# Kernel optimization log

Measured on AMD Instinct MI355X. Metric: run time of the kernel, lower is better.

## Reference

```python
import jax, jax.numpy as jnp
import numpy as np

N_NODES = 100000
N_EDGES = 1600000
IN_DIM = 128
HID = 32
HEADS = 4
OUT_DIM = 40
NEG_SLOPE = 0.2
BN_EPS = 1e-5


def setup_inputs() -> dict:
    key = jax.random.key(0)
    ks = jax.random.split(key, 13)
    x = jax.random.normal(ks[0], (N_NODES, IN_DIM), jnp.float32)
    edge_index = jax.random.randint(ks[1], (2, N_EDGES), 0, N_NODES, dtype=jnp.int32)
    s0 = 1.0 / np.sqrt(IN_DIM)
    s1 = 1.0 / np.sqrt(HEADS * HID)
    return {
        "x": x,
        "edge_index": edge_index,
        # layer 0: GATConv(IN_DIM -> HID, HEADS heads, concat)
        "W0": jax.random.normal(ks[2], (IN_DIM, HEADS * HID), jnp.float32) * s0,
        "a_src0": jax.random.normal(ks[3], (HEADS, HID), jnp.float32) * s0,
        "a_dst0": jax.random.normal(ks[4], (HEADS, HID), jnp.float32) * s0,
        "b0": jnp.zeros((HEADS * HID,), jnp.float32),
        # BatchNorm1d(HEADS*HID)
        "gamma0": jnp.ones((HEADS * HID,), jnp.float32),
        "beta0": jnp.zeros((HEADS * HID,), jnp.float32),
        # layer 1: GATConv(HEADS*HID -> OUT_DIM, 1 head, mean)
        "W1": jax.random.normal(ks[5], (HEADS * HID, OUT_DIM), jnp.float32) * s1,
        "a_src1": jax.random.normal(ks[6], (1, OUT_DIM), jnp.float32) * s1,
        "a_dst1": jax.random.normal(ks[7], (1, OUT_DIM), jnp.float32) * s1,
        "b1": jnp.zeros((OUT_DIM,), jnp.float32),
    }


def gat_conv(x, src, dst, n_nodes, W, a_src, a_dst, b, heads, concat):
    # linear transform: [N, H, C]
    h = (x @ W).reshape(n_nodes, heads, -1)
    # per-node attention logits [N, H]
    alpha_src = (h * a_src).sum(-1)
    alpha_dst = (h * a_dst).sum(-1)
    # per-edge raw attention [E, H]
    e = jax.nn.leaky_relu(alpha_src[src] + alpha_dst[dst], NEG_SLOPE)
    # softmax over incoming edges of each destination node
    m = jax.ops.segment_max(e, dst, num_segments=n_nodes)  # self-loops -> no empty segment
    ex = jnp.exp(e - m[dst])
    den = jax.ops.segment_sum(ex, dst, num_segments=n_nodes)
    # weighted scatter-aggregate of messages [E, H, C] -> [N, H, C]
    out = jax.ops.segment_sum(ex[:, :, None] * h[src], dst, num_segments=n_nodes)
    out = out / den[:, :, None]
    out = out.reshape(n_nodes, -1) if concat else out.mean(axis=1)
    return out + b


def batch_norm(x, gamma, beta):
    mu = x.mean(axis=0)
    var = x.var(axis=0)
    return (x - mu) * jax.lax.rsqrt(var + BN_EPS) * gamma + beta


def reference(x, edge_index, W0, a_src0, a_dst0, b0, gamma0, beta0,
              W1, a_src1, a_dst1, b1):
    n = x.shape[0]
    loop = jnp.arange(n, dtype=edge_index.dtype)
    src = jnp.concatenate([edge_index[0], loop])  # add self-loops (PyG default)
    dst = jnp.concatenate([edge_index[1], loop])
    # layer 0: GATConv -> BN -> ELU (dropout p=0 / eval -> identity)
    h = gat_conv(x, src, dst, n, W0, a_src0, a_dst0, b0, HEADS, True)
    h = jax.nn.elu(batch_norm(h, gamma0, beta0))
    # layer 1: GATConv, 1 head, mean aggregation, no BN/act
    out = gat_conv(h, src, dst, n, W1, a_src1, a_dst1, b1, 1, False)
    return out
```

## Files before the change

### kernel.cpp

```cpp
#include <hip/hip_runtime.h>
#include <hip/hip_bf16.h>
#include <math.h>

#define NN   100000
#define EE   1600000
#define ETOT (NN + EE)
#define IND  128
#define HD   128
#define OD   40
#define NEG  0.2f
#define BNEPS 1e-5f
#define NBKT 16

typedef __attribute__((ext_vector_type(8))) short bf16x8;
typedef __attribute__((ext_vector_type(4))) float f32x4;

__device__ __forceinline__ float lrelu(float x) { return x > 0.f ? x : NEG * x; }

__device__ __forceinline__ unsigned pack_bf16(float a, float b) {
  unsigned ua = __float_as_uint(a), ub = __float_as_uint(b);
  ua = (ua + 0x7fffu + ((ua >> 16) & 1u)) >> 16;
  ub = (ub + 0x7fffu + ((ub >> 16) & 1u)) >> 16;
  return ua | (ub << 16);
}
__device__ __forceinline__ float bf16_lo(unsigned v) { return __uint_as_float(v << 16); }
__device__ __forceinline__ float bf16_hi(unsigned v) { return __uint_as_float(v & 0xffff0000u); }

__global__ void prep_kernel(const float* __restrict__ W0, unsigned* __restrict__ w0t,
                            const int* __restrict__ ei, int* __restrict__ deg,
                            int* __restrict__ rank) {
  int gid = blockIdx.x * blockDim.x + threadIdx.x;
  if (gid < 128 * 64) {
    int n = gid & 127, kp = gid >> 7;
    float lo = W0[(size_t)(2 * kp) * 128 + n];
    float hi = W0[(size_t)(2 * kp + 1) * 128 + n];
    w0t[n * 64 + kp] = pack_bf16(lo, hi);
  }
  int i8 = gid * 8;
  if (i8 >= ETOT) return;
  int4 dA, dB;
  if (i8 < EE) {
    dA = *(const int4*)&ei[EE + i8];
    dB = *(const int4*)&ei[EE + i8 + 4];
  } else {
    int b = i8 - EE;
    dA = make_int4(b, b + 1, b + 2, b + 3);
    dB = make_int4(b + 4, b + 5, b + 6, b + 7);
  }
  int4 rA, rB;
  rA.x = atomicAdd(&deg[dA.x], 1);
  rA.y = atomicAdd(&deg[dA.y], 1);
  rA.z = atomicAdd(&deg[dA.z], 1);
  rA.w = atomicAdd(&deg[dA.w], 1);
  rB.x = atomicAdd(&deg[dB.x], 1);
  rB.y = atomicAdd(&deg[dB.y], 1);
  rB.z = atomicAdd(&deg[dB.z], 1);
  rB.w = atomicAdd(&deg[dB.w], 1);
  *(int4*)&rank[i8] = rA;
  *(int4*)&rank[i8 + 4] = rB;
}

__global__ __launch_bounds__(256) void gemm0_kernel(const float* __restrict__ x,
                                                    const unsigned* __restrict__ w0t,
                                                    const float* __restrict__ a_src0,
                                                    const float* __restrict__ a_dst0,
                                                    unsigned* __restrict__ h0b,
                                                    float* __restrict__ asrc0,
                                                    float* __restrict__ adst0) {
  __shared__ __align__(16) unsigned As[64][68];
  __shared__ __align__(16) unsigned Wt[128][68];
  int t = threadIdx.x;
  int rowbase = blockIdx.x * 64;
  for (int idx = t; idx < 128 * 64; idx += 256) {
    Wt[idx >> 6][idx & 63] = w0t[idx];
  }
  for (int idx = t; idx < 64 * 64; idx += 256) {
    int row = idx >> 6, kp = idx & 63;
    int r = rowbase + row;
    int rc = r < NN ? r : NN - 1;
    float2 v = *(const float2*)&x[(size_t)rc * 128 + kp * 2];
    As[row][kp] = pack_bf16(v.x, v.y);
  }
  __syncthreads();

  int lane = t & 63, w = t >> 6;
  int mrow = lane & 15, g = lane >> 4;
  f32x4 acc[8];
#pragma unroll
  for (int nt = 0; nt < 8; nt++) acc[nt] = (f32x4){0.f, 0.f, 0.f, 0.f};
#pragma unroll
  for (int ks = 0; ks < 4; ks++) {
    bf16x8 a = *(const bf16x8*)&As[w * 16 + mrow][ks * 16 + g * 4];
#pragma unroll
    for (int nt = 0; nt < 8; nt++) {
      bf16x8 b = *(const bf16x8*)&Wt[nt * 16 + mrow][ks * 16 + g * 4];
      acc[nt] = __builtin_amdgcn_mfma_f32_16x16x32_bf16(a, b, acc[nt], 0, 0, 0);
    }
  }
  int col = lane & 15;
  float as_[8], ad_[8];
#pragma unroll
  for (int nt = 0; nt < 8; nt++) {
    as_[nt] = a_src0[nt * 16 + col];
    ad_[nt] = a_dst0[nt * 16 + col];
  }
#pragma unroll
  for (int reg = 0; reg < 4; reg++) {
    int r = rowbase + w * 16 + g * 4 + reg;
    bool rok = r < NN;
    float hs0 = acc[0][reg] * as_[0] + acc[1][reg] * as_[1];
    float hs1 = acc[2][reg] * as_[2] + acc[3][reg] * as_[3];
    float hs2 = acc[4][reg] * as_[4] + acc[5][reg] * as_[5];
    float hs3 = acc[6][reg] * as_[6] + acc[7][reg] * as_[7];
    float hd0 = acc[0][reg] * ad_[0] + acc[1][reg] * ad_[1];
    float hd1 = acc[2][reg] * ad_[2] + acc[3][reg] * ad_[3];
    float hd2 = acc[4][reg] * ad_[4] + acc[5][reg] * ad_[5];
    float hd3 = acc[6][reg] * ad_[6] + acc[7][reg] * ad_[7];
#pragma unroll
    for (int mk = 1; mk < 16; mk <<= 1) {
      hs0 += __shfl_xor(hs0, mk); hs1 += __shfl_xor(hs1, mk);
      hs2 += __shfl_xor(hs2, mk); hs3 += __shfl_xor(hs3, mk);
      hd0 += __shfl_xor(hd0, mk); hd1 += __shfl_xor(hd1, mk);
      hd2 += __shfl_xor(hd2, mk); hd3 += __shfl_xor(hd3, mk);
    }
    if ((lane & 15) == 0 && rok) {
      asrc0[r * 4 + 0] = hs0; asrc0[r * 4 + 1] = hs1;
      asrc0[r * 4 + 2] = hs2; asrc0[r * 4 + 3] = hs3;
      adst0[r * 4 + 0] = hd0; adst0[r * 4 + 1] = hd1;
      adst0[r * 4 + 2] = hd2; adst0[r * 4 + 3] = hd3;
    }
#pragma unroll
    for (int nt = 0; nt < 8; nt++) {
      float v = acc[nt][reg];
      float nv = __shfl_xor(v, 1);
      if (!(col & 1) && rok) h0b[(size_t)r * 64 + nt * 8 + (col >> 1)] = pack_bf16(v, nv);
    }
  }
}

__global__ __launch_bounds__(256) void scanA_kernel(const int* __restrict__ deg,
                                                    int* __restrict__ scanned,
                                                    int* __restrict__ blocksums) {
  __shared__ int s[256];
  int t = threadIdx.x;
  int i = blockIdx.x * 256 + t;
  int v = (i < NN) ? deg[i] : 0;
  s[t] = v;
  __syncthreads();
  for (int off = 1; off < 256; off <<= 1) {
    int add = (t >= off) ? s[t - off] : 0;
    __syncthreads();
    s[t] += add;
    __syncthreads();
  }
  if (i < NN) scanned[i] = s[t];
  if (t == 255) blocksums[blockIdx.x] = s[255];
}

__global__ __launch_bounds__(512) void scanB_kernel(int* __restrict__ blocksums, int NB) {
  __shared__ int s[512];
  int t = threadIdx.x;
  int v = (t < NB) ? blocksums[t] : 0;
  s[t] = v;
  __syncthreads();
  for (int off = 1; off < 512; off <<= 1) {
    int add = (t >= off) ? s[t - off] : 0;
    __syncthreads();
    s[t] += add;
    __syncthreads();
  }
  if (t < NB) blocksums[t] = s[t] - v;
}

__global__ __launch_bounds__(256) void scanC_kernel(const int* __restrict__ scanned,
                                                    const int* __restrict__ deg,
                                                    const int* __restrict__ blocksums,
                                                    int* __restrict__ rowptr) {
  int i = blockIdx.x * 256 + threadIdx.x;
  if (i < NN) rowptr[i] = blocksums[blockIdx.x] + scanned[i] - deg[i];
  if (i == 0) rowptr[NN] = ETOT;
}

__global__ void scatter_kernel(const int* __restrict__ ei, const int* __restrict__ rowptr,
                               const int* __restrict__ rank, int* __restrict__ csr_src) {
  int i8 = (blockIdx.x * blockDim.x + threadIdx.x) * 8;
  if (i8 >= ETOT) return;
  int4 sA, dA, sB, dB;
  if (i8 < EE) {
    sA = *(const int4*)&ei[i8];
    sB = *(const int4*)&ei[i8 + 4];
    dA = *(const int4*)&ei[EE + i8];
    dB = *(const int4*)&ei[EE + i8 + 4];
  } else {
    int b = i8 - EE;
    sA = make_int4(b, b + 1, b + 2, b + 3);
    sB = make_int4(b + 4, b + 5, b + 6, b + 7);
    dA = sA; dB = sB;
  }
  int4 rA = *(const int4*)&rank[i8];
  int4 rB = *(const int4*)&rank[i8 + 4];
  int p0 = rowptr[dA.x] + rA.x;
  int p1 = rowptr[dA.y] + rA.y;
  int p2 = rowptr[dA.z] + rA.z;
  int p3 = rowptr[dA.w] + rA.w;
  int p4 = rowptr[dB.x] + rB.x;
  int p5 = rowptr[dB.y] + rB.y;
  int p6 = rowptr[dB.z] + rB.z;
  int p7 = rowptr[dB.w] + rB.w;
  csr_src[p0] = sA.x;
  csr_src[p1] = sA.y;
  csr_src[p2] = sA.z;
  csr_src[p3] = sA.w;
  csr_src[p4] = sB.x;
  csr_src[p5] = sB.y;
  csr_src[p6] = sB.z;
  csr_src[p7] = sB.w;
}

__global__ __launch_bounds__(256) void agg0_kernel(const int* __restrict__ csr_src,
                                                   const int* __restrict__ rowptr,
                                                   const float* __restrict__ asrc0,
                                                   const float* __restrict__ adst0,
                                                   const unsigned* __restrict__ h0b,
                                                   const float* __restrict__ b0,
                                                   unsigned* __restrict__ agg0b,
                                                   float* __restrict__ bnsumB,
                                                   float* __restrict__ bnsqB) {
  __shared__ float ws[16][4][17];
  __shared__ int   ss[16][16];
  __shared__ float Lsum[4][16][8], Lsq[4][16][8];
  int t = threadIdx.x;
  int grp = t >> 4;
  int p   = t & 15;
  int n = blockIdx.x * 16 + grp;
  int start = rowptr[n], end = rowptr[n + 1];
  float4 ad = *(const float4*)&adst0[(size_t)n * 4];
  int head = p >> 2;
  float a0 = 0.f, a1 = 0.f, a2 = 0.f, a3 = 0.f, a4 = 0.f, a5 = 0.f, a6 = 0.f, a7 = 0.f;
  float d0 = 0.f, d1 = 0.f, d2 = 0.f, d3 = 0.f;

  for (int base = start; base < end; base += 16) {
    int cnt = min(16, end - base);
    if (p < cnt) {
      int s = csr_src[base + p];
      float4 as = *(const float4*)&asrc0[(size_t)s * 4];
      float w0 = __expf(lrelu(as.x + ad.x));
      float w1 = __expf(lrelu(as.y + ad.y));
      float w2 = __expf(lrelu(as.z + ad.z));
      float w3 = __expf(lrelu(as.w + ad.w));
      d0 += w0; d1 += w1; d2 += w2; d3 += w3;
      ss[grp][p] = s;
      ws[grp][0][p] = w0;
      ws[grp][1][p] = w1;
      ws[grp][2][p] = w2;
      ws[grp][3][p] = w3;
    }
    __builtin_amdgcn_wave_barrier();
    for (int eb = 0; eb < cnt; eb += 4) {
      int e0 = eb, e1 = eb + 1, e2 = eb + 2, e3 = eb + 3;
      float w0 = ws[grp][head][e0];
      float w1 = (e1 < cnt) ? ws[grp][head][e1] : 0.f;
      float w2 = (e2 < cnt) ? ws[grp][head][e2] : 0.f;
      float w3 = (e3 < cnt) ? ws[grp][head][e3] : 0.f;
      int s0 = ss[grp][e0];
      int s1 = ss[grp][(e1 < cnt) ? e1 : e0];
      int s2 = ss[grp][(e2 < cnt) ? e2 : e0];
      int s3 = ss[grp][(e3 < cnt) ? e3 : e0];
      uint4 h0v = *(const uint4*)&h0b[(size_t)s0 * 64 + p * 4];
      uint4 h1v = *(const uint4*)&h0b[(size_t)s1 * 64 + p * 4];
      uint4 h2v = *(const uint4*)&h0b[(size_t)s2 * 64 + p * 4];
      uint4 h3v = *(const uint4*)&h0b[(size_t)s3 * 64 + p * 4];
      a0 += w0 * bf16_lo(h0v.x); a1 += w0 * bf16_hi(h0v.x);
      a2 += w0 * bf16_lo(h0v.y); a3 += w0 * bf16_hi(h0v.y);
      a4 += w0 * bf16_lo(h0v.z); a5 += w0 * bf16_hi(h0v.z);
      a6 += w0 * bf16_lo(h0v.w); a7 += w0 * bf16_hi(h0v.w);
      a0 += w1 * bf16_lo(h1v.x); a1 += w1 * bf16_hi(h1v.x);
      a2 += w1 * bf16_lo(h1v.y); a3 += w1 * bf16_hi(h1v.y);
      a4 += w1 * bf16_lo(h1v.z); a5 += w1 * bf16_hi(h1v.z);
      a6 += w1 * bf16_lo(h1v.w); a7 += w1 * bf16_hi(h1v.w);
      a0 += w2 * bf16_lo(h2v.x); a1 += w2 * bf16_hi(h2v.x);
      a2 += w2 * bf16_lo(h2v.y); a3 += w2 * bf16_hi(h2v.y);
      a4 += w2 * bf16_lo(h2v.z); a5 += w2 * bf16_hi(h2v.z);
      a6 += w2 * bf16_lo(h2v.w); a7 += w2 * bf16_hi(h2v.w);
      a0 += w3 * bf16_lo(h3v.x); a1 += w3 * bf16_hi(h3v.x);
      a2 += w3 * bf16_lo(h3v.y); a3 += w3 * bf16_hi(h3v.y);
      a4 += w3 * bf16_lo(h3v.z); a5 += w3 * bf16_hi(h3v.z);
      a6 += w3 * bf16_lo(h3v.w); a7 += w3 * bf16_hi(h3v.w);
    }
    __builtin_amdgcn_wave_barrier();
  }
#pragma unroll
  for (int mk = 1; mk < 16; mk <<= 1) {
    d0 += __shfl_xor(d0, mk);
    d1 += __shfl_xor(d1, mk);
    d2 += __shfl_xor(d2, mk);
    d3 += __shfl_xor(d3, mk);
  }
  float dh = head == 0 ? d0 : head == 1 ? d1 : head == 2 ? d2 : d3;
  float rd = 1.f / dh;
  int c = p * 8;
  float4 b1v = *(const float4*)&b0[c];
  float4 b2v = *(const float4*)&b0[c + 4];
  float o0 = a0 * rd + b1v.x, o1 = a1 * rd + b1v.y;
  float o2 = a2 * rd + b1v.z, o3 = a3 * rd + b1v.w;
  float o4 = a4 * rd + b2v.x, o5 = a5 * rd + b2v.y;
  float o6 = a6 * rd + b2v.z, o7 = a7 * rd + b2v.w;
  uint4 o;
  o.x = pack_bf16(o0, o1);
  o.y = pack_bf16(o2, o3);
  o.z = pack_bf16(o4, o5);
  o.w = pack_bf16(o6, o7);
  *(uint4*)&agg0b[(size_t)n * 64 + p * 4] = o;

  float s0 = o0, s1 = o1, s2 = o2, s3 = o3, s4 = o4, s5 = o5, s6 = o6, s7 = o7;
  float q0 = o0 * o0, q1 = o1 * o1, q2 = o2 * o2, q3 = o3 * o3;
  float q4 = o4 * o4, q5 = o5 * o5, q6 = o6 * o6, q7 = o7 * o7;
#pragma unroll
  for (int mk = 16; mk < 64; mk <<= 1) {
    s0 += __shfl_xor(s0, mk); s1 += __shfl_xor(s1, mk);
    s2 += __shfl_xor(s2, mk); s3 += __shfl_xor(s3, mk);
    s4 += __shfl_xor(s4, mk); s5 += __shfl_xor(s5, mk);
    s6 += __shfl_xor(s6, mk); s7 += __shfl_xor(s7, mk);
    q0 += __shfl_xor(q0, mk); q1 += __shfl_xor(q1, mk);
    q2 += __shfl_xor(q2, mk); q3 += __shfl_xor(q3, mk);
    q4 += __shfl_xor(q4, mk); q5 += __shfl_xor(q5, mk);
    q6 += __shfl_xor(q6, mk); q7 += __shfl_xor(q7, mk);
  }
  int lane = t & 63, wv = t >> 6;
  if (lane < 16) {
    Lsum[wv][lane][0] = s0; Lsum[wv][lane][1] = s1;
    Lsum[wv][lane][2] = s2; Lsum[wv][lane][3] = s3;
    Lsum[wv][lane][4] = s4; Lsum[wv][lane][5] = s5;
    Lsum[wv][lane][6] = s6; Lsum[wv][lane][7] = s7;
    Lsq[wv][lane][0] = q0; Lsq[wv][lane][1] = q1;
    Lsq[wv][lane][2] = q2; Lsq[wv][lane][3] = q3;
    Lsq[wv][lane][4] = q4; Lsq[wv][lane][5] = q5;
    Lsq[wv][lane][6] = q6; Lsq[wv][lane][7] = q7;
  }
  __syncthreads();
  if (t < 128) {
    int pp = t >> 3, jj = t & 7;
    float s = Lsum[0][pp][jj] + Lsum[1][pp][jj] + Lsum[2][pp][jj] + Lsum[3][pp][jj];
    float q = Lsq[0][pp][jj] + Lsq[1][pp][jj] + Lsq[2][pp][jj] + Lsq[3][pp][jj];
    int bkt = blockIdx.x & (NBKT - 1);
    atomicAdd(&bnsumB[bkt * 128 + t], s);
    atomicAdd(&bnsqB[bkt * 128 + t], q);
  }
}

__global__ __launch_bounds__(256) void gemm1_kernel(const unsigned* __restrict__ agg0b,
                                                    const float* __restrict__ bnsumB,
                                                    const float* __restrict__ bnsqB,
                                                    const float* __restrict__ gamma,
                                                    const float* __restrict__ beta,
                                                    const float* __restrict__ W1,
                                                    const float* __restrict__ a_src1,
                                                    const float* __restrict__ a_dst1,
                                                    unsigned* __restrict__ h1b,
                                                    float* __restrict__ asrc1,
                                                    float* __restrict__ adst1) {
  __shared__ __align__(16) unsigned As[64][68];
  __shared__ __align__(16) unsigned Wt[48][68];
  __shared__ float bnsc[128], bnsh[128];
  int t = threadIdx.x;
  int rowbase = blockIdx.x * 64;

  if (t < 128) {
    float s = 0.f, q = 0.f;
#pragma unroll
    for (int k = 0; k < NBKT; k++) {
      s += bnsumB[k * 128 + t];
      q += bnsqB[k * 128 + t];
    }
    float mu = s / (float)NN;
    float var = q / (float)NN - mu * mu;
    float sc = gamma[t] / sqrtf(var + BNEPS);
    bnsc[t] = sc;
    bnsh[t] = beta[t] - mu * sc;
  }
  for (int idx = t; idx < 48 * 64; idx += 256) {
    int c = idx >> 6, kp = idx & 63;
    float lo = (c < OD) ? W1[(size_t)(2 * kp) * OD + c] : 0.f;
    float hi = (c < OD) ? W1[(size_t)(2 * kp + 1) * OD + c] : 0.f;
    Wt[c][kp] = pack_bf16(lo, hi);
  }
  __syncthreads();
  for (int idx = t; idx < 64 * 16; idx += 256) {
    int row = idx >> 4, c4 = idx & 15;
    int r = rowbase + row;
    int rc = r < NN ? r : NN - 1;
    int k = c4 * 8;
    uint4 hv = *(const uint4*)&agg0b[(size_t)rc * 64 + c4 * 4];
    float y0 = bf16_lo(hv.x) * bnsc[k + 0] + bnsh[k + 0];
    float y1 = bf16_hi(hv.x) * bnsc[k + 1] + bnsh[k + 1];
    float y2 = bf16_lo(hv.y) * bnsc[k + 2] + bnsh[k + 2];
    float y3 = bf16_hi(hv.y) * bnsc[k + 3] + bnsh[k + 3];
    float y4 = bf16_lo(hv.z) * bnsc[k + 4] + bnsh[k + 4];
    float y5 = bf16_hi(hv.z) * bnsc[k + 5] + bnsh[k + 5];
    float y6 = bf16_lo(hv.w) * bnsc[k + 6] + bnsh[k + 6];
    float y7 = bf16_hi(hv.w) * bnsc[k + 7] + bnsh[k + 7];
    y0 = y0 > 0.f ? y0 : expm1f(y0);
    y1 = y1 > 0.f ? y1 : expm1f(y1);
    y2 = y2 > 0.f ? y2 : expm1f(y2);
    y3 = y3 > 0.f ? y3 : expm1f(y3);
    y4 = y4 > 0.f ? y4 : expm1f(y4);
    y5 = y5 > 0.f ? y5 : expm1f(y5);
    y6 = y6 > 0.f ? y6 : expm1f(y6);
    y7 = y7 > 0.f ? y7 : expm1f(y7);
    As[row][c4 * 4 + 0] = pack_bf16(y0, y1);
    As[row][c4 * 4 + 1] = pack_bf16(y2, y3);
    As[row][c4 * 4 + 2] = pack_bf16(y4, y5);
    As[row][c4 * 4 + 3] = pack_bf16(y6, y7);
  }
  __syncthreads();

  int lane = t & 63, w = t >> 6;
  int mrow = lane & 15, g = lane >> 4;
  f32x4 acc0 = {0.f, 0.f, 0.f, 0.f};
  f32x4 acc1 = {0.f, 0.f, 0.f, 0.f};
  f32x4 acc2 = {0.f, 0.f, 0.f, 0.f};
#pragma unroll
  for (int ks = 0; ks < 4; ks++) {
    bf16x8 a = *(const bf16x8*)&As[w * 16 + mrow][ks * 16 + g * 4];
    bf16x8 b0v = *(const bf16x8*)&Wt[mrow][ks * 16 + g * 4];
    bf16x8 b1v = *(const bf16x8*)&Wt[16 + mrow][ks * 16 + g * 4];
    bf16x8 b2v = *(const bf16x8*)&Wt[32 + mrow][ks * 16 + g * 4];
    acc0 = __builtin_amdgcn_mfma_f32_16x16x32_bf16(a, b0v, acc0, 0, 0, 0);
    acc1 = __builtin_amdgcn_mfma_f32_16x16x32_bf16(a, b1v, acc1, 0, 0, 0);
    acc2 = __builtin_amdgcn_mfma_f32_16x16x32_bf16(a, b2v, acc2, 0, 0, 0);
  }
  int col = lane & 15;
  float as0 = (col < OD)      ? a_src1[col]      : 0.f;
  float as1 = (16 + col < OD) ? a_src1[16 + col] : 0.f;
  float as2 = (32 + col < OD) ? a_src1[32 + col] : 0.f;
  float ad0 = (col < OD)      ? a_dst1[col]      : 0.f;
  float ad1 = (16 + col < OD) ? a_dst1[16 + col] : 0.f;
  float ad2 = (32 + col < OD) ? a_dst1[32 + col] : 0.f;
#pragma unroll
  for (int reg = 0; reg < 4; reg++) {
    int r = rowbase + w * 16 + g * 4 + reg;
    float v0 = acc0[reg], v1 = acc1[reg], v2 = acc2[reg];
    float ps = v0 * as0 + v1 * as1 + v2 * as2;
    float pd = v0 * ad0 + v1 * ad1 + v2 * ad2;
#pragma unroll
    for (int mk = 1; mk < 16; mk <<= 1) { ps += __shfl_xor(ps, mk); pd += __shfl_xor(pd, mk); }
    bool rok = r < NN;
    if ((lane & 15) == 0 && rok) { asrc1[r] = ps; adst1[r] = pd; }
    float n0 = __shfl_xor(v0, 1), n1 = __shfl_xor(v1, 1), n2 = __shfl_xor(v2, 1);
    if (!(col & 1) && rok) {
      h1b[(size_t)r * 20 + ((col) >> 1)]      = pack_bf16(v0, n0);
      h1b[(size_t)r * 20 + ((16 + col) >> 1)] = pack_bf16(v1, n1);
      if (32 + col < OD) h1b[(size_t)r * 20 + ((32 + col) >> 1)] = pack_bf16(v2, n2);
    }
  }
}

__global__ __launch_bounds__(256) void agg1_kernel(const int* __restrict__ csr_src,
                                                   const int* __restrict__ rowptr,
                                                   const float* __restrict__ asrc1,
                                                   const float* __restrict__ adst1,
                                                   const unsigned* __restrict__ h1b,
                                                   const float* __restrict__ b1,
                                                   float* __restrict__ out) {
  __shared__ float ws[4][64];
  __shared__ int   ss[4][64];
  int t = threadIdx.x;
  int lane = t & 63, wv = t >> 6;
  int n = blockIdx.x * 4 + wv;
  if (n >= NN) return;
  int start = rowptr[n], end = rowptr[n + 1];
  float ad = adst1[n];
  int esub = lane / 10;
  int c2   = lane - esub * 10;
  float dsum = 0.f;
  float acc0 = 0.f, acc1 = 0.f, acc2 = 0.f, acc3 = 0.f;
  for (int base = start; base < end; base += 64) {
    int cnt = min(64, end - base);
    if (lane < cnt) {
      int s = csr_src[base + lane];
      float w = __expf(lrelu(asrc1[s] + ad));
      dsum += w;
      ss[wv][lane] = s;
      ws[wv][lane] = w;
    }
    __builtin_amdgcn_wave_barrier();
    if (lane < 60) {
      int e = esub;
      for (; e + 18 < cnt; e += 24) {
        int s0 = ss[wv][e], s1 = ss[wv][e + 6], s2 = ss[wv][e + 12], s3 = ss[wv][e + 18];
        uint2 u0 = *(const uint2*)&h1b[(size_t)s0 * 20 + c2 * 2];
        uint2 u1 = *(const uint2*)&h1b[(size_t)s1 * 20 + c2 * 2];
        uint2 u2 = *(const uint2*)&h1b[(size_t)s2 * 20 + c2 * 2];
        uint2 u3 = *(const uint2*)&h1b[(size_t)s3 * 20 + c2 * 2];
        float w0 = ws[wv][e], w1 = ws[wv][e + 6], w2 = ws[wv][e + 12], w3 = ws[wv][e + 18];
        acc0 += w0 * bf16_lo(u0.x); acc1 += w0 * bf16_hi(u0.x);
        acc2 += w0 * bf16_lo(u0.y); acc3 += w0 * bf16_hi(u0.y);
        acc0 += w1 * bf16_lo(u1.x); acc1 += w1 * bf16_hi(u1.x);
        acc2 += w1 * bf16_lo(u1.y); acc3 += w1 * bf16_hi(u1.y);
        acc0 += w2 * bf16_lo(u2.x); acc1 += w2 * bf16_hi(u2.x);
        acc2 += w2 * bf16_lo(u2.y); acc3 += w2 * bf16_hi(u2.y);
        acc0 += w3 * bf16_lo(u3.x); acc1 += w3 * bf16_hi(u3.x);
        acc2 += w3 * bf16_lo(u3.y); acc3 += w3 * bf16_hi(u3.y);
      }
      for (; e < cnt; e += 6) {
        int s = ss[wv][e];
        float w = ws[wv][e];
        uint2 u = *(const uint2*)&h1b[(size_t)s * 20 + c2 * 2];
        acc0 += w * bf16_lo(u.x); acc1 += w * bf16_hi(u.x);
        acc2 += w * bf16_lo(u.y); acc3 += w * bf16_hi(u.y);
      }
    }
    __builtin_amdgcn_wave_barrier();
  }
#pragma unroll
  for (int mk = 1; mk < 64; mk <<= 1) dsum += __shfl_xor(dsum, mk);
  float rd = 1.f / dsum;
  float p01 = __shfl(acc0, lane + 10), p02 = __shfl(acc0, lane + 20);
  float p03 = __shfl(acc0, lane + 30), p04 = __shfl(acc0, lane + 40);
  float p05 = __shfl(acc0, lane + 50);
  float p11 = __shfl(acc1, lane + 10), p12 = __shfl(acc1, lane + 20);
  float p13 = __shfl(acc1, lane + 30), p14 = __shfl(acc1, lane + 40);
  float p15 = __shfl(acc1, lane + 50);
  float p21 = __shfl(acc2, lane + 10), p22 = __shfl(acc2, lane + 20);
  float p23 = __shfl(acc2, lane + 30), p24 = __shfl(acc2, lane + 40);
  float p25 = __shfl(acc2, lane + 50);
  float p31 = __shfl(acc3, lane + 10), p32 = __shfl(acc3, lane + 20);
  float p33 = __shfl(acc3, lane + 30), p34 = __shfl(acc3, lane + 40);
  float p35 = __shfl(acc3, lane + 50);
  if (lane < 10) {
    float t0 = acc0 + p01 + p02 + p03 + p04 + p05;
    float t1 = acc1 + p11 + p12 + p13 + p14 + p15;
    float t2 = acc2 + p21 + p22 + p23 + p24 + p25;
    float t3 = acc3 + p31 + p32 + p33 + p34 + p35;
    float4 bv = *(const float4*)&b1[lane * 4];
    float4 o;
    o.x = t0 * rd + bv.x;
    o.y = t1 * rd + bv.y;
    o.z = t2 * rd + bv.z;
    o.w = t3 * rd + bv.w;
    *(float4*)&out[(size_t)n * 40 + lane * 4] = o;
  }
}

extern "C" void kernel_launch(void* const* d_in, const int* in_sizes, int n_in,
                              void* d_out, int out_size, void* d_ws, size_t ws_size,
                              hipStream_t stream) {
  const float* x       = (const float*)d_in[0];
  const int*   ei      = (const int*)d_in[1];
  const float* W0      = (const float*)d_in[2];
  const float* a_src0  = (const float*)d_in[3];
  const float* a_dst0  = (const float*)d_in[4];
  const float* b0      = (const float*)d_in[5];
  const float* gamma0  = (const float*)d_in[6];
  const float* beta0   = (const float*)d_in[7];
  const float* W1      = (const float*)d_in[8];
  const float* a_src1  = (const float*)d_in[9];
  const float* a_dst1  = (const float*)d_in[10];
  const float* b1      = (const float*)d_in[11];
  float* out = (float*)d_out;

  char* ws = (char*)d_ws;
  size_t off = 0;
  auto alloc = [&](size_t bytes) {
    void* p = ws + off;
    off += (bytes + 255) & ~(size_t)255;
    return p;
  };
  int*   deg      = (int*)alloc((size_t)NN * 4);
  float* bnsumB   = (float*)alloc(NBKT * 128 * 4);
  float* bnsqB    = (float*)alloc(NBKT * 128 * 4);
  unsigned* h0b   = (unsigned*)alloc((size_t)NN * 64 * 4);
  unsigned* agg0b = (unsigned*)alloc((size_t)NN * 64 * 4);
  unsigned* h1b   = (unsigned*)alloc((size_t)NN * 20 * 4);
  float* asrc0    = (float*)alloc((size_t)NN * 4 * 4);
  float* adst0    = (float*)alloc((size_t)NN * 4 * 4);
  float* asrc1    = (float*)alloc((size_t)NN * 4);
  float* adst1    = (float*)alloc((size_t)NN * 4);
  int*   rowptr   = (int*)alloc((size_t)(NN + 1) * 4);
  int*   scanned  = (int*)alloc((size_t)NN * 4);
  int*   csr      = (int*)alloc((size_t)ETOT * 4);
  int*   rank     = (int*)alloc((size_t)ETOT * 4);
  int*   bsums    = (int*)alloc(512 * 4);
  unsigned* w0t   = (unsigned*)alloc(128 * 64 * 4);
  (void)ws_size; (void)in_sizes; (void)n_in; (void)out_size;

  size_t zbytes = (char*)(bnsqB + NBKT * 128) - (char*)deg;
  hipMemsetAsync(deg, 0, zbytes, stream);

  const int NB = (NN + 255) / 256;
  const int e8grid = (ETOT / 8 + 255) / 256;

  prep_kernel<<<e8grid, 256, 0, stream>>>(W0, w0t, ei, deg, rank);
  gemm0_kernel<<<(NN + 63) / 64, 256, 0, stream>>>(x, w0t, a_src0, a_dst0, h0b, asrc0, adst0);
  scanA_kernel<<<NB, 256, 0, stream>>>(deg, scanned, bsums);
  scanB_kernel<<<1, 512, 0, stream>>>(bsums, NB);
  scanC_kernel<<<NB, 256, 0, stream>>>(scanned, deg, bsums, rowptr);
  scatter_kernel<<<e8grid, 256, 0, stream>>>(ei, rowptr, rank, csr);
  agg0_kernel<<<NN / 16, 256, 0, stream>>>(csr, rowptr, asrc0, adst0, h0b, b0, agg0b,
                                           bnsumB, bnsqB);
  gemm1_kernel<<<(NN + 63) / 64, 256, 0, stream>>>(agg0b, bnsumB, bnsqB, gamma0, beta0,
                                                   W1, a_src1, a_dst1, h1b, asrc1, adst1);
  agg1_kernel<<<(NN + 3) / 4, 256, 0, stream>>>(csr, rowptr, asrc1, adst1, h1b, b1, out);
}
```

Baseline: 301.9 us.

## Fuse degree counting and layer-0 GEMM into one interleaved kernel

Merges the prep kernel (W0 transpose/pack and degree atomics) with the layer-0 GEMM into a single launch. Blocks are interleaved in groups of three: two do GEMM tiles and one does degree counting, so atomic-heavy work overlaps with MFMA work. Each GEMM block now repacks W0 to bf16 itself from global memory instead of reading a pre-packed buffer. That removes one launch and the intermediate buffer but adds redundant per-block packing work and strided W0 reads.

Result: faster. 280.5 us (-7.1%).

```diff
diff --git a/kernel.cpp b/kernel.cpp
--- a/kernel.cpp
+++ b/kernel.cpp
@@ -12,6 +12,11 @@
 #define BNEPS 1e-5f
 #define NBKT 16
 
+#define NGEMM ((NN + 63) / 64)
+#define NDEG  ((ETOT / 8 + 255) / 256)
+#define NTRIPLE 831
+#define NFUSED (NTRIPLE * 3)
+
 typedef __attribute__((ext_vector_type(8))) short bf16x8;
 typedef __attribute__((ext_vector_type(4))) float f32x4;
 
@@ -26,53 +31,57 @@
 __device__ __forceinline__ float bf16_lo(unsigned v) { return __uint_as_float(v << 16); }
 __device__ __forceinline__ float bf16_hi(unsigned v) { return __uint_as_float(v & 0xffff0000u); }
 
-__global__ void prep_kernel(const float* __restrict__ W0, unsigned* __restrict__ w0t,
-                            const int* __restrict__ ei, int* __restrict__ deg,
-                            int* __restrict__ rank) {
-  int gid = blockIdx.x * blockDim.x + threadIdx.x;
-  if (gid < 128 * 64) {
-    int n = gid & 127, kp = gid >> 7;
+__global__ __launch_bounds__(256) void fused0_kernel(const float* __restrict__ x,
+                                                     const float* __restrict__ W0,
+                                                     const float* __restrict__ a_src0,
+                                                     const float* __restrict__ a_dst0,
+                                                     unsigned* __restrict__ h0b,
+                                                     float* __restrict__ asrc0,
+                                                     float* __restrict__ adst0,
+                                                     const int* __restrict__ ei,
+                                                     int* __restrict__ deg,
+                                                     int* __restrict__ rank) {
+  __shared__ __align__(16) unsigned As[64][68];
+  __shared__ __align__(16) unsigned Wt[128][68];
+  int bid = blockIdx.x;
+  int trip = bid / 3, rem = bid - trip * 3;
+  int t = threadIdx.x;
+
+  if (rem == 2) {
+    int i8 = (trip * 256 + t) * 8;
+    if (i8 >= ETOT) return;
+    int4 dA, dB;
+    if (i8 < EE) {
+      dA = *(const int4*)&ei[EE + i8];
+      dB = *(const int4*)&ei[EE + i8 + 4];
+    } else {
+      int b = i8 - EE;
+      dA = make_int4(b, b + 1, b + 2, b + 3);
+      dB = make_int4(b + 4, b + 5, b + 6, b + 7);
+    }
+    int4 rA, rB;
+    rA.x = atomicAdd(&deg[dA.x], 1);
+    rA.y = atomicAdd(&deg[dA.y], 1);
+    rA.z = atomicAdd(&deg[dA.z], 1);
+    rA.w = atomicAdd(&deg[dA.w], 1);
+    rB.x = atomicAdd(&deg[dB.x], 1);
+    rB.y = atomicAdd(&deg[dB.y], 1);
+    rB.z = atomicAdd(&deg[dB.z], 1);
+    rB.w = atomicAdd(&deg[dB.w], 1);
+    *(int4*)&rank[i8] = rA;
+    *(int4*)&rank[i8 + 4] = rB;
+    return;
+  }
+
+  int gb = trip * 2 + rem;
+  if (gb >= NGEMM) return;
+  int rowbase = gb * 64;
+
+  for (int idx = t; idx < 128 * 64; idx += 256) {
+    int kp = idx >> 7, n = idx & 127;
     float lo = W0[(size_t)(2 * kp) * 128 + n];
     float hi = W0[(size_t)(2 * kp + 1) * 128 + n];
-    w0t[n * 64 + kp] = pack_bf16(lo, hi);
-  }
-  int i8 = gid * 8;
-  if (i8 >= ETOT) return;
-  int4 dA, dB;
-  if (i8 < EE) {
-    dA = *(const int4*)&ei[EE + i8];
-    dB = *(const int4*)&ei[EE + i8 + 4];
-  } else {
-    int b = i8 - EE;
-    dA = make_int4(b, b + 1, b + 2, b + 3);
-    dB = make_int4(b + 4, b + 5, b + 6, b + 7);
-  }
-  int4 rA, rB;
-  rA.x = atomicAdd(&deg[dA.x], 1);
-  rA.y = atomicAdd(&deg[dA.y], 1);
-  rA.z = atomicAdd(&deg[dA.z], 1);
-  rA.w = atomicAdd(&deg[dA.w], 1);
-  rB.x = atomicAdd(&deg[dB.x], 1);
-  rB.y = atomicAdd(&deg[dB.y], 1);
-  rB.z = atomicAdd(&deg[dB.z], 1);
-  rB.w = atomicAdd(&deg[dB.w], 1);
-  *(int4*)&rank[i8] = rA;
-  *(int4*)&rank[i8 + 4] = rB;
-}
-
-__global__ __launch_bounds__(256) void gemm0_kernel(const float* __restrict__ x,
-                                                    const unsigned* __restrict__ w0t,
-                                                    const float* __restrict__ a_src0,
-                                                    const float* __restrict__ a_dst0,
-                                                    unsigned* __restrict__ h0b,
-                                                    float* __restrict__ asrc0,
-                                                    float* __restrict__ adst0) {
-  __shared__ __align__(16) unsigned As[64][68];
-  __shared__ __align__(16) unsigned Wt[128][68];
-  int t = threadIdx.x;
-  int rowbase = blockIdx.x * 64;
-  for (int idx = t; idx < 128 * 64; idx += 256) {
-    Wt[idx >> 6][idx & 63] = w0t[idx];
+    Wt[n][kp] = pack_bf16(lo, hi);
   }
   for (int idx = t; idx < 64 * 64; idx += 256) {
     int row = idx >> 6, kp = idx & 63;
@@ -581,7 +590,6 @@
   int*   csr      = (int*)alloc((size_t)ETOT * 4);
   int*   rank     = (int*)alloc((size_t)ETOT * 4);
   int*   bsums    = (int*)alloc(512 * 4);
-  unsigned* w0t   = (unsigned*)alloc(128 * 64 * 4);
   (void)ws_size; (void)in_sizes; (void)n_in; (void)out_size;
 
   size_t zbytes = (char*)(bnsqB + NBKT * 128) - (char*)deg;
@@ -590,8 +598,8 @@
   const int NB = (NN + 255) / 256;
   const int e8grid = (ETOT / 8 + 255) / 256;
 
-  prep_kernel<<<e8grid, 256, 0, stream>>>(W0, w0t, ei, deg, rank);
-  gemm0_kernel<<<(NN + 63) / 64, 256, 0, stream>>>(x, w0t, a_src0, a_dst0, h0b, asrc0, adst0);
+  fused0_kernel<<<NFUSED, 256, 0, stream>>>(x, W0, a_src0, a_dst0, h0b, asrc0, adst0,
+                                            ei, deg, rank);
   scanA_kernel<<<NB, 256, 0, stream>>>(deg, scanned, bsums);
   scanB_kernel<<<1, 512, 0, stream>>>(bsums, NB);
   scanC_kernel<<<NB, 256, 0, stream>>>(scanned, deg, bsums, rowptr);
```
